# Kernel tuning notes

Hardware: AMD Instinct MI355X
Metric: run time of the kernel (lower is better)

Reference implementation:

```python
import jax, jax.numpy as jnp
import numpy as np

N = 50000
D_IN = 256
OUT = 16
HEADS = 32
GAT_C = OUT  # out_channels + beta_on(=0)


def _gat_conv(x, src, dst, W, att_src, att_dst, bias):
    """PyG GATConv, concat=False (mean over heads), with self-loops already appended."""
    n = x.shape[0]
    xp = (x @ W).reshape(n, HEADS, GAT_C)            # [N,H,C]
    a_s = jnp.einsum('nhc,hc->nh', xp, att_src)       # [N,H]
    a_d = jnp.einsum('nhc,hc->nh', xp, att_dst)       # [N,H]
    e = jax.nn.leaky_relu(a_s[src] + a_d[dst], 0.2)   # [E,H]
    # segment softmax over incoming edges of each dst node
    m = jax.ops.segment_max(e, dst, num_segments=n)
    e = jnp.exp(e - m[dst])
    s = jax.ops.segment_sum(e, dst, num_segments=n)
    alpha = e / (s[dst] + 1e-16)                      # [E,H]
    out = jax.ops.segment_sum(alpha[:, :, None] * xp[src], dst, num_segments=n)  # [N,H,C]
    return out.mean(axis=1) + bias                    # [N,C]


def setup_inputs() -> dict:
    key = jax.random.key(0)
    ks = jax.random.split(key, 16)
    E = 800000
    x = jax.random.normal(ks[0], (N, D_IN), dtype=jnp.float32)
    edge_index = jax.random.randint(ks[1], (2, E), 0, N, dtype=jnp.int64)
    sc = 1.0 / np.sqrt(D_IN)
    W1 = jax.random.normal(ks[2], (D_IN, HEADS * GAT_C), dtype=jnp.float32) * sc
    att_src1 = jax.random.normal(ks[3], (HEADS, GAT_C), dtype=jnp.float32) * 0.1
    att_dst1 = jax.random.normal(ks[4], (HEADS, GAT_C), dtype=jnp.float32) * 0.1
    b1 = jnp.zeros((GAT_C,), dtype=jnp.float32)
    W2 = jax.random.normal(ks[5], (D_IN, HEADS * GAT_C), dtype=jnp.float32) * sc
    att_src2 = jax.random.normal(ks[6], (HEADS, GAT_C), dtype=jnp.float32) * 0.1
    att_dst2 = jax.random.normal(ks[7], (HEADS, GAT_C), dtype=jnp.float32) * 0.1
    b2 = jnp.zeros((GAT_C,), dtype=jnp.float32)
    lin1_w = jax.random.normal(ks[8], (D_IN, 4 * OUT), dtype=jnp.float32) * sc
    lin1_b = jnp.zeros((4 * OUT,), dtype=jnp.float32)
    lin2_w = jax.random.normal(ks[9], (4 * OUT, OUT), dtype=jnp.float32) * (1.0 / np.sqrt(4 * OUT))
    lin2_b = jnp.zeros((OUT,), dtype=jnp.float32)
    return {"x": x, "edge_index": edge_index,
            "W1": W1, "att_src1": att_src1, "att_dst1": att_dst1, "b1": b1,
            "W2": W2, "att_src2": att_src2, "att_dst2": att_dst2, "b2": b2,
            "lin1_w": lin1_w, "lin1_b": lin1_b, "lin2_w": lin2_w, "lin2_b": lin2_b}


def reference(x, edge_index, W1, att_src1, att_dst1, b1, W2, att_src2, att_dst2, b2,
              lin1_w, lin1_b, lin2_w, lin2_b):
    n = x.shape[0]
    loops = jnp.arange(n, dtype=edge_index.dtype)
    # conv1: flow source_to_target on edge_index -> aggregate src=row0 into dst=row1
    src = jnp.concatenate([edge_index[0], loops])
    dst = jnp.concatenate([edge_index[1], loops])
    x_in = jax.nn.elu(_gat_conv(x, src, dst, W1, att_src1, att_dst1, b1))
    # conv2: flow target_to_source on transposed edge_index -> same effective (src,dst)
    x_out = jax.nn.elu(_gat_conv(x, src, dst, W2, att_src2, att_dst2, b2))
    x1 = jax.nn.elu(x @ lin1_w + lin1_b)
    x_self = jax.nn.elu(x1 @ lin2_w + lin2_b)
    return (x_in, x_out, x_self)
```

## Files before the change

### kernel.cpp

```cpp
#include <hip/hip_runtime.h>

typedef __bf16 bf16x8 __attribute__((ext_vector_type(8)));
typedef float  f32x4  __attribute__((ext_vector_type(4)));
typedef float  f32x2  __attribute__((ext_vector_type(2)));

#define NNODES   50000
#define DIN      256
#define HEADS    32
#define CDIM     16
#define NH       512
#define ERAW     800000
#define SCAN_B   196
#define LDSW     280
#define LOG2E    1.4426950408889634f
#define CAST_B   12500
#define PREP_B   (CAST_B + SCAN_B + 18)

#if __has_builtin(__builtin_amdgcn_exp2f)
#define EXP2(x) __builtin_amdgcn_exp2f(x)
#else
#define EXP2(x) __expf((x) * 0.6931471805599453f)
#endif

__device__ __forceinline__ float b2f(unsigned short u) {
    return __uint_as_float(((unsigned)u) << 16);
}
__device__ __forceinline__ unsigned short f2b(float f) {
    unsigned v = __float_as_uint(f);
    v += 0x7fffu + ((v >> 16) & 1u);
    return (unsigned short)(v >> 16);
}

__global__ void __launch_bounds__(256) k_prep(
        const float* __restrict__ x, unsigned short* __restrict__ xb,
        const float* __restrict__ W0, const float* __restrict__ W1,
        const float* __restrict__ w1, const float* __restrict__ w2,
        unsigned short* __restrict__ Wt2, unsigned short* __restrict__ w1t,
        unsigned short* __restrict__ w2t,
        const int* __restrict__ ei, int* __restrict__ flag,
        int* __restrict__ deg, int* __restrict__ cur) {
    __shared__ unsigned short T[64][258];
    int bid = blockIdx.x, t = threadIdx.x;

    if (bid < CAST_B) {
        int i = bid * 256 + t;
        float4 v = *(const float4*)(x + (size_t)i * 4);
        ushort4 o;
        o.x = f2b(v.x); o.y = f2b(v.y); o.z = f2b(v.z); o.w = f2b(v.w);
        *(ushort4*)(xb + (size_t)i * 4) = o;
        return;
    }
    if (bid < CAST_B + SCAN_B) {
        int i = (bid - CAST_B) * 256 + t;
        if (i < NNODES) { deg[i] = 0; cur[i] = 0; }
        if (bid == CAST_B && t == 0) {
            int nz = 0;
            #pragma unroll
            for (int k = 0; k < 64; ++k) nz |= ei[2 * k + 1];
            flag[0] = (nz == 0) ? 1 : 0;
        }
        return;
    }
    int tb = bid - (CAST_B + SCAN_B);
    if (tb == 17) {
        for (int idx = t; idx < 1024; idx += 256) {
            int n = idx >> 6, k = idx & 63;
            w2t[n * 64 + k] = f2b(w2[k * CDIM + n]);
        }
        return;
    }
    const float* src; unsigned short* dst; int srcStride, doPi, tile;
    if (tb < 8)       { src = W0; dst = Wt2;             srcStride = NH; doPi = 1; tile = tb; }
    else if (tb < 16) { src = W1; dst = Wt2 + 512 * DIN; srcStride = NH; doPi = 1; tile = tb - 8; }
    else              { src = w1; dst = w1t;             srcStride = 64; doPi = 0; tile = 0; }
    int n0 = tile * 64;
    int nl = (t & 15) * 4;
    int kr = t >> 4;
    for (int kk = 0; kk < 256; kk += 16) {
        int k = kk + kr;
        float4 v = *(const float4*)(src + (size_t)k * srcStride + n0 + nl);
        T[nl + 0][k] = f2b(v.x);
        T[nl + 1][k] = f2b(v.y);
        T[nl + 2][k] = f2b(v.z);
        T[nl + 3][k] = f2b(v.w);
    }
    __syncthreads();
    int rl = t >> 2;
    int pr = doPi ? (((rl & 15) << 2) | (rl >> 4)) : rl;
    #pragma unroll
    for (int j = 0; j < 16; ++j) {
        int c4 = (t & 3) + 4 * j;
        ushort2 o0 = *(const ushort2*)&T[pr][c4 * 4];
        ushort2 o1 = *(const ushort2*)&T[pr][c4 * 4 + 2];
        ushort4 o; o.x = o0.x; o.y = o0.y; o.z = o1.x; o.w = o1.y;
        *(ushort4*)(dst + ((size_t)(n0 + rl)) * DIN + c4 * 4) = o;
    }
}

__global__ void k_hist(const int* __restrict__ ei, const int* __restrict__ flag,
                       int* __restrict__ deg) {
    int e = blockIdx.x * 256 + threadIdx.x;
    int d = flag[0] ? ei[2 * ERAW + 2 * e] : ei[ERAW + e];
    atomicAdd(&deg[d], 1);
}

__global__ void k_scan_blk(const int* __restrict__ deg, int* __restrict__ part,
                           int* __restrict__ bsum) {
    __shared__ int sm[256];
    int b = blockIdx.x, t = threadIdx.x, i = b * 256 + t;
    int v = (i < NNODES) ? deg[i] : 0;
    sm[t] = v; __syncthreads();
    for (int off = 1; off < 256; off <<= 1) {
        int u = (t >= off) ? sm[t - off] : 0;
        __syncthreads();
        sm[t] += u; __syncthreads();
    }
    if (i < NNODES) part[i] = sm[t] - v;
    if (t == 255) bsum[b] = sm[255];
}

__global__ void k_scan_top(int* __restrict__ bsum) {
    __shared__ int sm[256];
    int t = threadIdx.x;
    int v = (t < SCAN_B) ? bsum[t] : 0;
    sm[t] = v; __syncthreads();
    for (int off = 1; off < 256; off <<= 1) {
        int u = (t >= off) ? sm[t - off] : 0;
        __syncthreads();
        sm[t] += u; __syncthreads();
    }
    if (t < SCAN_B) bsum[t] = sm[t] - v;
}

__global__ void k_scatter(const int* __restrict__ ei, const int* __restrict__ flag,
                          const int* __restrict__ part, const int* __restrict__ bsum,
                          int* __restrict__ cur, int* __restrict__ csr) {
    int e = blockIdx.x * 256 + threadIdx.x;
    int s, d;
    if (flag[0]) { s = ei[2 * e]; d = ei[2 * ERAW + 2 * e]; }
    else         { s = ei[e];     d = ei[ERAW + e]; }
    int pos = part[d] + bsum[d >> 8] + atomicAdd(&cur[d], 1);
    csr[pos] = s;
}

__global__ void __launch_bounds__(256)
k_gemm_xp(const unsigned short* __restrict__ xb,
          const unsigned short* __restrict__ Wt,
          unsigned* __restrict__ xp8,
          const float* __restrict__ att_src, const float* __restrict__ att_dst,
          float* __restrict__ a_s, float* __restrict__ a_d) {
    __shared__ unsigned short As[64 * LDSW];
    int row0 = blockIdx.x * 64;
    int tid = threadIdx.x;
    int w = tid >> 6, lane = tid & 63;
    int r = lane & 15, quad = lane >> 4;

    {
        int row = tid >> 2, slot = tid & 3;
        const uint4* g = (const uint4*)(xb + (size_t)(row0 + row) * DIN);
        uint4* l = (uint4*)(As + row * LDSW);
        #pragma unroll
        for (int i = 0; i < 8; ++i)
            l[slot + 4 * i] = g[slot + 4 * i];
    }
    __syncthreads();

    const f32x4* As4 = (const f32x4*)att_src;
    const f32x4* Ad4 = (const f32x4*)att_dst;

    #pragma unroll
    for (int ch = 0; ch < 2; ++ch) {
        f32x4 acc[4][4] = {};
        #pragma unroll
        for (int kc = 0; kc < 8; ++kc) {
            bf16x8 a[4], b[4];
            #pragma unroll
            for (int sub = 0; sub < 4; ++sub)
                a[sub] = *(const bf16x8*)(As + (sub * 16 + r) * LDSW + kc * 32 + quad * 8);
            #pragma unroll
            for (int t = 0; t < 4; ++t) {
                int col = ch * 256 + w * 64 + t * 16 + r;
                b[t] = *(const bf16x8*)(Wt + (size_t)col * DIN + kc * 32 + quad * 8);
            }
            #pragma unroll
            for (int t = 0; t < 4; ++t)
                #pragma unroll
                for (int sub = 0; sub < 4; ++sub)
                    acc[sub][t] = __builtin_amdgcn_mfma_f32_16x16x32_bf16(a[sub], b[t], acc[sub][t], 0, 0, 0);
        }
        int h = ch * 16 + w * 4 + (r >> 2);
        f32x4 sc = As4[h * 4 + (r & 3)];
        f32x4 dc = Ad4[h * 4 + (r & 3)];
        #pragma unroll
        for (int sub = 0; sub < 4; ++sub) {
            #pragma unroll
            for (int j = 0; j < 4; ++j) {
                int row = row0 + sub * 16 + quad * 4 + j;
                if (row < NNODES) {
                    unsigned u = (unsigned)__builtin_amdgcn_cvt_pk_fp8_f32(
                                     acc[sub][0][j], acc[sub][1][j], 0, false);
                    u = (unsigned)__builtin_amdgcn_cvt_pk_fp8_f32(
                                     acc[sub][2][j], acc[sub][3][j], (int)u, true);
                    xp8[(size_t)row * 128 + ch * 64 + w * 16 + r] = u;
                }
            }
            f32x4 ps = acc[sub][0] * sc.x + acc[sub][1] * sc.y
                     + acc[sub][2] * sc.z + acc[sub][3] * sc.w;
            f32x4 pd = acc[sub][0] * dc.x + acc[sub][1] * dc.y
                     + acc[sub][2] * dc.z + acc[sub][3] * dc.w;
            #pragma unroll
            for (int m = 1; m <= 2; m <<= 1) {
                #pragma unroll
                for (int c = 0; c < 4; ++c) {
                    ps[c] += __shfl_xor(ps[c], m, 64);
                    pd[c] += __shfl_xor(pd[c], m, 64);
                }
            }
            int j = r & 3;
            int row = row0 + sub * 16 + quad * 4 + j;
            if (row < NNODES) {
                a_s[row * HEADS + h] = ps[j] * LOG2E;
                a_d[row * HEADS + h] = pd[j] * LOG2E;
            }
        }
    }
}

__global__ void k_conv(const int* __restrict__ csr, const int* __restrict__ part,
                       const int* __restrict__ bsum, const int* __restrict__ deg,
                       const unsigned* __restrict__ xp8,
                       const float* __restrict__ a_s, const float* __restrict__ a_d,
                       const float* __restrict__ bias, float* __restrict__ out) {
    int nd = blockIdx.x * 4 + (threadIdx.x >> 6);
    int ln = threadIdx.x & 63;
    int h  = ln >> 1;
    int cb = (ln & 1) * 8;
    float adn = a_d[nd * HEADS + h];
    int beg = __builtin_amdgcn_readfirstlane(part[nd])
            + __builtin_amdgcn_readfirstlane(bsum[nd >> 8]);
    int cnt = __builtin_amdgcn_readfirstlane(deg[nd]);
    const uint2* xv = (const uint2*)xp8;

    float denom = 0.f;
    float acc[8] = {0, 0, 0, 0, 0, 0, 0, 0};

    #define EDGE_BODY(AV, QV, LIVE)                                        \
    {                                                                      \
        float tt = (AV) + adn;                                             \
        tt = fmaxf(tt, 0.2f * tt);                                         \
        float e = EXP2(tt);                                                \
        e = (LIVE) ? e : 0.f;                                              \
        denom += e;                                                        \
        f32x2 p0 = __builtin_amdgcn_cvt_pk_f32_fp8((int)(QV).x, false);    \
        f32x2 p1 = __builtin_amdgcn_cvt_pk_f32_fp8((int)(QV).x, true);     \
        f32x2 p2 = __builtin_amdgcn_cvt_pk_f32_fp8((int)(QV).y, false);    \
        f32x2 p3 = __builtin_amdgcn_cvt_pk_f32_fp8((int)(QV).y, true);     \
        acc[0] += e * p0.x; acc[1] += e * p0.y;                            \
        acc[2] += e * p1.x; acc[3] += e * p1.y;                            \
        acc[4] += e * p2.x; acc[5] += e * p2.y;                            \
        acc[6] += e * p3.x; acc[7] += e * p3.y;                            \
    }

    float avS = a_s[nd * HEADS + h];
    uint2 qvS = xv[(size_t)nd * 64 + ln];
    int nb = (cnt + 3) >> 2;
    float avP[4]; uint2 qvP[4]; int svN[4];
    if (nb > 0) {
        #pragma unroll
        for (int k = 0; k < 4; ++k) {
            int ce = k < cnt ? k : cnt - 1;
            int s = csr[beg + ce];
            avP[k] = a_s[s * HEADS + h];
            qvP[k] = xv[(size_t)s * 64 + ln];
        }
        #pragma unroll
        for (int k = 0; k < 4; ++k) {
            int idx = 4 + k;
            int ce = idx < cnt ? idx : cnt - 1;
            svN[k] = csr[beg + ce];
        }
    }
    __builtin_amdgcn_sched_barrier(0);
    EDGE_BODY(avS, qvS, 1)

    for (int b = 1; b < nb; ++b) {
        float avN[4]; uint2 qvN[4];
        #pragma unroll
        for (int k = 0; k < 4; ++k) {
            int s = svN[k];
            avN[k] = a_s[s * HEADS + h];
            qvN[k] = xv[(size_t)s * 64 + ln];
        }
        {
            int nbase = (b + 1 < nb ? b + 1 : nb - 1) * 4;
            #pragma unroll
            for (int k = 0; k < 4; ++k) {
                int idx = nbase + k;
                int ce = idx < cnt ? idx : cnt - 1;
                svN[k] = csr[beg + ce];
            }
        }
        __builtin_amdgcn_sched_barrier(0);
        #pragma unroll
        for (int k = 0; k < 4; ++k) EDGE_BODY(avP[k], qvP[k], 1)
        #pragma unroll
        for (int k = 0; k < 4; ++k) { avP[k] = avN[k]; qvP[k] = qvN[k]; }
    }
    if (nb > 0) {
        #pragma unroll
        for (int k = 0; k < 4; ++k) {
            int idx = (nb - 1) * 4 + k;
            EDGE_BODY(avP[k], qvP[k], idx < cnt)
        }
    }
    #undef EDGE_BODY

    float inv = 1.f / (denom + 1e-16f);
    #pragma unroll
    for (int c = 0; c < 8; ++c) acc[c] *= inv;

    #pragma unroll
    for (int mask = 2; mask <= 32; mask <<= 1) {
        #pragma unroll
        for (int c = 0; c < 8; ++c) acc[c] += __shfl_xor(acc[c], mask, 64);
    }
    if (ln < 2) {
        #pragma unroll
        for (int c2 = 0; c2 < 8; ++c2) {
            int c = cb + c2;
            float o = acc[c2] * (1.0f / HEADS) + bias[c];
            out[(size_t)nd * CDIM + c] = o > 0.f ? o : expm1f(o);
        }
    }
}

__global__ void __launch_bounds__(256)
k_mlp(const unsigned short* __restrict__ xb, const unsigned short* __restrict__ w1t,
      const float* __restrict__ bb1, const unsigned short* __restrict__ w2t,
      const float* __restrict__ bb2, float* __restrict__ out) {
    __shared__ unsigned short T[4][64][72];
    int wv = threadIdx.x >> 6;
    int wave = blockIdx.x * 4 + wv;
    if (wave >= 782) return;
    int lane = threadIdx.x & 63;
    int r = lane & 15, quad = lane >> 4;
    int row0 = wave * 64;

    f32x4 acc[4][4] = {};
    #pragma unroll
    for (int kc = 0; kc < 8; ++kc) {
        bf16x8 a[4];
        #pragma unroll
        for (int sub = 0; sub < 4; ++sub) {
            int row = row0 + sub * 16 + r;
            if (row0 + sub * 16 < NNODES)
                a[sub] = *(const bf16x8*)(xb + (size_t)row * DIN + kc * 32 + quad * 8);
            else {
                union { unsigned short u[8]; bf16x8 v; } z;
                #pragma unroll
                for (int j = 0; j < 8; ++j) z.u[j] = 0;
                a[sub] = z.v;
            }
        }
        #pragma unroll
        for (int t = 0; t < 4; ++t) {
            int col = t * 16 + r;
            bf16x8 b = *(const bf16x8*)(w1t + (size_t)col * DIN + kc * 32 + quad * 8);
            #pragma unroll
            for (int sub = 0; sub < 4; ++sub)
                acc[sub][t] = __builtin_amdgcn_mfma_f32_16x16x32_bf16(a[sub], b, acc[sub][t], 0, 0, 0);
        }
    }
    #pragma unroll
    for (int sub = 0; sub < 4; ++sub) {
        #pragma unroll
        for (int t = 0; t < 4; ++t) {
            int col = t * 16 + r;
            float bv = bb1[col];
            #pragma unroll
            for (int j = 0; j < 4; ++j) {
                float v = acc[sub][t][j] + bv;
                v = v > 0.f ? v : expm1f(v);
                T[wv][sub * 16 + quad * 4 + j][col] = f2b(v);
            }
        }
    }
    f32x4 acc2[4] = {};
    #pragma unroll
    for (int sub = 0; sub < 4; ++sub) {
        #pragma unroll
        for (int kc = 0; kc < 2; ++kc) {
            bf16x8 a = *(const bf16x8*)&T[wv][sub * 16 + r][kc * 32 + quad * 8];
            bf16x8 b = *(const bf16x8*)(w2t + r * 64 + kc * 32 + quad * 8);
            acc2[sub] = __builtin_amdgcn_mfma_f32_16x16x32_bf16(a, b, acc2[sub], 0, 0, 0);
        }
    }
    float bv2 = bb2[r];
    #pragma unroll
    for (int sub = 0; sub < 4; ++sub) {
        #pragma unroll
        for (int j = 0; j < 4; ++j) {
            int row = row0 + sub * 16 + quad * 4 + j;
            if (row < NNODES) {
                float v = acc2[sub][j] + bv2;
                out[(size_t)row * CDIM + r] = v > 0.f ? v : expm1f(v);
            }
        }
    }
}

extern "C" void kernel_launch(void* const* d_in, const int* in_sizes, int n_in,
                              void* d_out, int out_size, void* d_ws, size_t ws_size,
                              hipStream_t stream) {
    const float* x  = (const float*)d_in[0];
    const int* ei   = (const int*)d_in[1];
    const float* W[2]    = {(const float*)d_in[2], (const float*)d_in[6]};
    const float* atS[2]  = {(const float*)d_in[3], (const float*)d_in[7]};
    const float* atD[2]  = {(const float*)d_in[4], (const float*)d_in[8]};
    const float* bias[2] = {(const float*)d_in[5], (const float*)d_in[9]};
    const float* w1 = (const float*)d_in[10];
    const float* b1 = (const float*)d_in[11];
    const float* w2 = (const float*)d_in[12];
    const float* b2 = (const float*)d_in[13];
    float* out = (float*)d_out;

    char* ws = (char*)d_ws;
    unsigned* xp8 = (unsigned*)(ws);
    unsigned short* xb  = (unsigned short*)(ws + 25600000);
    unsigned short* Wt2 = (unsigned short*)(ws + 51200000);
    unsigned short* w1t = (unsigned short*)(ws + 51724288);
    unsigned short* w2t = (unsigned short*)(ws + 51757056);
    float* a_s = (float*)(ws + 51759104);
    float* a_d = (float*)(ws + 58159104);
    int* deg   = (int*)(ws + 64559104);
    int* cur   = (int*)(ws + 64759104);
    int* part  = (int*)(ws + 64959104);
    int* bsum  = (int*)(ws + 65159104);
    int* csr   = (int*)(ws + 65160128);
    int* flag  = (int*)(ws + 68360128);

    k_prep    <<<PREP_B, 256, 0, stream>>>(x, xb, W[0], W[1], w1, w2,
                                           Wt2, w1t, w2t, ei, flag, deg, cur);
    k_hist    <<<3125, 256, 0, stream>>>(ei, flag, deg);
    k_scan_blk<<<SCAN_B, 256, 0, stream>>>(deg, part, bsum);
    k_scan_top<<<1, 256, 0, stream>>>(bsum);
    k_scatter <<<3125, 256, 0, stream>>>(ei, flag, part, bsum, cur, csr);

    for (int cv = 0; cv < 2; ++cv) {
        k_gemm_xp<<<782, 256, 0, stream>>>(xb, Wt2 + (size_t)cv * 512 * DIN,
                                           xp8, atS[cv], atD[cv], a_s, a_d);
        k_conv   <<<12500, 256, 0, stream>>>(csr, part, bsum, deg, xp8, a_s, a_d,
                                             bias[cv], out + (size_t)cv * 800000);
    }
    k_mlp<<<196, 256, 0, stream>>>(xb, w1t, b1, w2t, b2, out + 1600000);
}
```

Measured before the change: 461.2 us.

## Merge GEMMs, histogram and MLP into one launch; fuse both convs and scan

Independent work (both GAT projection GEMMs, the degree histogram, and the MLP branch) now runs as block ranges of a single k_mix launch, so small kernels can overlap and fill the GPU. Both conv layers run in one 25000-block launch using separate xp8/a_s/a_d buffers. The two-level scan is merged into one kernel where the last-finishing block does the top-level scan, tracked by an atomic counter. This needs a larger workspace, so the old sequential path is kept as a fallback when the workspace is too small.

After: 445.9 us. -3.3%, faster.

```diff
diff --git a/kernel.cpp b/kernel.cpp
--- a/kernel.cpp
+++ b/kernel.cpp
@@ -15,6 +15,10 @@
 #define LOG2E    1.4426950408889634f
 #define CAST_B   12500
 #define PREP_B   (CAST_B + SCAN_B + 18)
+#define GEMM_B   782
+#define HIST_B   3125
+#define MLP_B    196
+#define MIX_B    (2 * GEMM_B + HIST_B + MLP_B)
 
 #if __has_builtin(__builtin_amdgcn_exp2f)
 #define EXP2(x) __builtin_amdgcn_exp2f(x)
@@ -58,6 +62,7 @@
             #pragma unroll
             for (int k = 0; k < 64; ++k) nz |= ei[2 * k + 1];
             flag[0] = (nz == 0) ? 1 : 0;
+            flag[1] = 0;
         }
         return;
     }
@@ -97,16 +102,222 @@
     }
 }
 
+__device__ __forceinline__ void hist_body(int bid, int t,
+        const int* __restrict__ ei, const int* __restrict__ flag,
+        int* __restrict__ deg) {
+    int e = bid * 256 + t;
+    int d = flag[0] ? ei[2 * ERAW + 2 * e] : ei[ERAW + e];
+    atomicAdd(&deg[d], 1);
+}
+
+__device__ __forceinline__ void gemm_body(int bid, int tid,
+        const unsigned short* __restrict__ xb,
+        const unsigned short* __restrict__ Wt,
+        unsigned* __restrict__ xp8,
+        const float* __restrict__ att_src, const float* __restrict__ att_dst,
+        float* __restrict__ a_s, float* __restrict__ a_d,
+        unsigned short* As) {
+    int row0 = bid * 64;
+    int w = tid >> 6, lane = tid & 63;
+    int r = lane & 15, quad = lane >> 4;
+
+    {
+        int row = tid >> 2, slot = tid & 3;
+        const uint4* g = (const uint4*)(xb + (size_t)(row0 + row) * DIN);
+        uint4* l = (uint4*)(As + row * LDSW);
+        #pragma unroll
+        for (int i = 0; i < 8; ++i)
+            l[slot + 4 * i] = g[slot + 4 * i];
+    }
+    __syncthreads();
+
+    const f32x4* As4 = (const f32x4*)att_src;
+    const f32x4* Ad4 = (const f32x4*)att_dst;
+
+    #pragma unroll
+    for (int ch = 0; ch < 2; ++ch) {
+        f32x4 acc[4][4] = {};
+        #pragma unroll
+        for (int kc = 0; kc < 8; ++kc) {
+            bf16x8 a[4], b[4];
+            #pragma unroll
+            for (int sub = 0; sub < 4; ++sub)
+                a[sub] = *(const bf16x8*)(As + (sub * 16 + r) * LDSW + kc * 32 + quad * 8);
+            #pragma unroll
+            for (int t = 0; t < 4; ++t) {
+                int col = ch * 256 + w * 64 + t * 16 + r;
+                b[t] = *(const bf16x8*)(Wt + (size_t)col * DIN + kc * 32 + quad * 8);
+            }
+            #pragma unroll
+            for (int t = 0; t < 4; ++t)
+                #pragma unroll
+                for (int sub = 0; sub < 4; ++sub)
+                    acc[sub][t] = __builtin_amdgcn_mfma_f32_16x16x32_bf16(a[sub], b[t], acc[sub][t], 0, 0, 0);
+        }
+        int h = ch * 16 + w * 4 + (r >> 2);
+        f32x4 sc = As4[h * 4 + (r & 3)];
+        f32x4 dc = Ad4[h * 4 + (r & 3)];
+        #pragma unroll
+        for (int sub = 0; sub < 4; ++sub) {
+            #pragma unroll
+            for (int j = 0; j < 4; ++j) {
+                int row = row0 + sub * 16 + quad * 4 + j;
+                if (row < NNODES) {
+                    unsigned u = (unsigned)__builtin_amdgcn_cvt_pk_fp8_f32(
+                                     acc[sub][0][j], acc[sub][1][j], 0, false);
+                    u = (unsigned)__builtin_amdgcn_cvt_pk_fp8_f32(
+                                     acc[sub][2][j], acc[sub][3][j], (int)u, true);
+                    xp8[(size_t)row * 128 + ch * 64 + w * 16 + r] = u;
+                }
+            }
+            f32x4 ps = acc[sub][0] * sc.x + acc[sub][1] * sc.y
+                     + acc[sub][2] * sc.z + acc[sub][3] * sc.w;
+            f32x4 pd = acc[sub][0] * dc.x + acc[sub][1] * dc.y
+                     + acc[sub][2] * dc.z + acc[sub][3] * dc.w;
+            #pragma unroll
+            for (int m = 1; m <= 2; m <<= 1) {
+                #pragma unroll
+                for (int c = 0; c < 4; ++c) {
+                    ps[c] += __shfl_xor(ps[c], m, 64);
+                    pd[c] += __shfl_xor(pd[c], m, 64);
+                }
+            }
+            int j = r & 3;
+            int row = row0 + sub * 16 + quad * 4 + j;
+            if (row < NNODES) {
+                a_s[row * HEADS + h] = ps[j] * LOG2E;
+                a_d[row * HEADS + h] = pd[j] * LOG2E;
+            }
+        }
+    }
+}
+
+__device__ __forceinline__ void mlp_body(int bid, int tid,
+        const unsigned short* __restrict__ xb, const unsigned short* __restrict__ w1t,
+        const float* __restrict__ bb1, const unsigned short* __restrict__ w2t,
+        const float* __restrict__ bb2, float* __restrict__ out,
+        unsigned short* Tbase) {
+    int wv = tid >> 6;
+    int wave = bid * 4 + wv;
+    if (wave >= GEMM_B) return;
+    unsigned short* T = Tbase + wv * 64 * 72;
+    int lane = tid & 63;
+    int r = lane & 15, quad = lane >> 4;
+    int row0 = wave * 64;
+
+    f32x4 acc[4][4] = {};
+    #pragma unroll
+    for (int kc = 0; kc < 8; ++kc) {
+        bf16x8 a[4];
+        #pragma unroll
+        for (int sub = 0; sub < 4; ++sub) {
+            int row = row0 + sub * 16 + r;
+            if (row0 + sub * 16 < NNODES)
+                a[sub] = *(const bf16x8*)(xb + (size_t)row * DIN + kc * 32 + quad * 8);
+            else {
+                union { unsigned short u[8]; bf16x8 v; } z;
+                #pragma unroll
+                for (int j = 0; j < 8; ++j) z.u[j] = 0;
+                a[sub] = z.v;
+            }
+        }
+        #pragma unroll
+        for (int t = 0; t < 4; ++t) {
+            int col = t * 16 + r;
+            bf16x8 b = *(const bf16x8*)(w1t + (size_t)col * DIN + kc * 32 + quad * 8);
+            #pragma unroll
+            for (int sub = 0; sub < 4; ++sub)
+                acc[sub][t] = __builtin_amdgcn_mfma_f32_16x16x32_bf16(a[sub], b, acc[sub][t], 0, 0, 0);
+        }
+    }
+    #pragma unroll
+    for (int sub = 0; sub < 4; ++sub) {
+        #pragma unroll
+        for (int t = 0; t < 4; ++t) {
+            int col = t * 16 + r;
+            float bv = bb1[col];
+            #pragma unroll
+            for (int j = 0; j < 4; ++j) {
+                float v = acc[sub][t][j] + bv;
+                v = v > 0.f ? v : expm1f(v);
+                T[(sub * 16 + quad * 4 + j) * 72 + col] = f2b(v);
+            }
+        }
+    }
+    f32x4 acc2[4] = {};
+    #pragma unroll
+    for (int sub = 0; sub < 4; ++sub) {
+        #pragma unroll
+        for (int kc = 0; kc < 2; ++kc) {
+            bf16x8 a = *(const bf16x8*)&T[(sub * 16 + r) * 72 + kc * 32 + quad * 8];
+            bf16x8 b = *(const bf16x8*)(w2t + r * 64 + kc * 32 + quad * 8);
+            acc2[sub] = __builtin_amdgcn_mfma_f32_16x16x32_bf16(a, b, acc2[sub], 0, 0, 0);
+        }
+    }
+    float bv2 = bb2[r];
+    #pragma unroll
+    for (int sub = 0; sub < 4; ++sub) {
+        #pragma unroll
+        for (int j = 0; j < 4; ++j) {
+            int row = row0 + sub * 16 + quad * 4 + j;
+            if (row < NNODES) {
+                float v = acc2[sub][j] + bv2;
+                out[(size_t)row * CDIM + r] = v > 0.f ? v : expm1f(v);
+            }
+        }
+    }
+}
+
 __global__ void k_hist(const int* __restrict__ ei, const int* __restrict__ flag,
                        int* __restrict__ deg) {
-    int e = blockIdx.x * 256 + threadIdx.x;
-    int d = flag[0] ? ei[2 * ERAW + 2 * e] : ei[ERAW + e];
-    atomicAdd(&deg[d], 1);
-}
-
-__global__ void k_scan_blk(const int* __restrict__ deg, int* __restrict__ part,
-                           int* __restrict__ bsum) {
+    hist_body(blockIdx.x, threadIdx.x, ei, flag, deg);
+}
+
+__global__ void __launch_bounds__(256)
+k_gemm_xp(const unsigned short* __restrict__ xb, const unsigned short* __restrict__ Wt,
+          unsigned* __restrict__ xp8,
+          const float* __restrict__ atS, const float* __restrict__ atD,
+          float* __restrict__ a_s, float* __restrict__ a_d) {
+    __shared__ unsigned short As[64 * LDSW];
+    gemm_body(blockIdx.x, threadIdx.x, xb, Wt, xp8, atS, atD, a_s, a_d, As);
+}
+
+__global__ void __launch_bounds__(256)
+k_mlp(const unsigned short* __restrict__ xb, const unsigned short* __restrict__ w1t,
+      const float* __restrict__ bb1, const unsigned short* __restrict__ w2t,
+      const float* __restrict__ bb2, float* __restrict__ out) {
+    __shared__ unsigned short T[4 * 64 * 72];
+    mlp_body(blockIdx.x, threadIdx.x, xb, w1t, bb1, w2t, bb2, out, T);
+}
+
+__global__ void __launch_bounds__(256) k_mix(
+        const unsigned short* __restrict__ xb, const unsigned short* __restrict__ Wt2,
+        unsigned* __restrict__ xp8_0, unsigned* __restrict__ xp8_1,
+        const float* __restrict__ atS0, const float* __restrict__ atD0,
+        const float* __restrict__ atS1, const float* __restrict__ atD1,
+        float* __restrict__ as0, float* __restrict__ ad0,
+        float* __restrict__ as1, float* __restrict__ ad1,
+        const int* __restrict__ ei, const int* __restrict__ flag,
+        int* __restrict__ deg,
+        const unsigned short* __restrict__ w1t, const float* __restrict__ b1,
+        const unsigned short* __restrict__ w2t, const float* __restrict__ b2,
+        float* __restrict__ outm) {
+    __shared__ unsigned short SH[4 * 64 * 72];
+    int bid = blockIdx.x, tid = threadIdx.x;
+    if (bid < GEMM_B)
+        gemm_body(bid, tid, xb, Wt2, xp8_0, atS0, atD0, as0, ad0, SH);
+    else if (bid < 2 * GEMM_B)
+        gemm_body(bid - GEMM_B, tid, xb, Wt2 + 512 * DIN, xp8_1, atS1, atD1, as1, ad1, SH);
+    else if (bid < 2 * GEMM_B + HIST_B)
+        hist_body(bid - 2 * GEMM_B, tid, ei, flag, deg);
+    else
+        mlp_body(bid - (2 * GEMM_B + HIST_B), tid, xb, w1t, b1, w2t, b2, outm, SH);
+}
+
+__global__ void k_scan(const int* __restrict__ deg, int* __restrict__ part,
+                       int* __restrict__ bsum, int* __restrict__ done) {
     __shared__ int sm[256];
+    __shared__ int isLast;
     int b = blockIdx.x, t = threadIdx.x, i = b * 256 + t;
     int v = (i < NNODES) ? deg[i] : 0;
     sm[t] = v; __syncthreads();
@@ -117,19 +328,20 @@
     }
     if (i < NNODES) part[i] = sm[t] - v;
     if (t == 255) bsum[b] = sm[255];
-}
-
-__global__ void k_scan_top(int* __restrict__ bsum) {
-    __shared__ int sm[256];
-    int t = threadIdx.x;
-    int v = (t < SCAN_B) ? bsum[t] : 0;
-    sm[t] = v; __syncthreads();
-    for (int off = 1; off < 256; off <<= 1) {
-        int u = (t >= off) ? sm[t - off] : 0;
-        __syncthreads();
-        sm[t] += u; __syncthreads();
-    }
-    if (t < SCAN_B) bsum[t] = sm[t] - v;
+    __threadfence();
+    if (t == 0) isLast = (atomicAdd(done, 1) == SCAN_B - 1);
+    __syncthreads();
+    if (isLast) {
+        __threadfence();
+        int v2 = (t < SCAN_B) ? bsum[t] : 0;
+        sm[t] = v2; __syncthreads();
+        for (int off = 1; off < 256; off <<= 1) {
+            int u = (t >= off) ? sm[t - off] : 0;
+            __syncthreads();
+            sm[t] += u; __syncthreads();
+        }
+        if (t < SCAN_B) bsum[t] = sm[t] - v2;
+    }
 }
 
 __global__ void k_scatter(const int* __restrict__ ei, const int* __restrict__ flag,
@@ -144,94 +356,20 @@
 }
 
 __global__ void __launch_bounds__(256)
-k_gemm_xp(const unsigned short* __restrict__ xb,
-          const unsigned short* __restrict__ Wt,
-          unsigned* __restrict__ xp8,
-          const float* __restrict__ att_src, const float* __restrict__ att_dst,
-          float* __restrict__ a_s, float* __restrict__ a_d) {
-    __shared__ unsigned short As[64 * LDSW];
-    int row0 = blockIdx.x * 64;
-    int tid = threadIdx.x;
-    int w = tid >> 6, lane = tid & 63;
-    int r = lane & 15, quad = lane >> 4;
-
-    {
-        int row = tid >> 2, slot = tid & 3;
-        const uint4* g = (const uint4*)(xb + (size_t)(row0 + row) * DIN);
-        uint4* l = (uint4*)(As + row * LDSW);
-        #pragma unroll
-        for (int i = 0; i < 8; ++i)
-            l[slot + 4 * i] = g[slot + 4 * i];
-    }
-    __syncthreads();
-
-    const f32x4* As4 = (const f32x4*)att_src;
-    const f32x4* Ad4 = (const f32x4*)att_dst;
-
-    #pragma unroll
-    for (int ch = 0; ch < 2; ++ch) {
-        f32x4 acc[4][4] = {};
-        #pragma unroll
-        for (int kc = 0; kc < 8; ++kc) {
-            bf16x8 a[4], b[4];
-            #pragma unroll
-            for (int sub = 0; sub < 4; ++sub)
-                a[sub] = *(const bf16x8*)(As + (sub * 16 + r) * LDSW + kc * 32 + quad * 8);
-            #pragma unroll
-            for (int t = 0; t < 4; ++t) {
-                int col = ch * 256 + w * 64 + t * 16 + r;
-                b[t] = *(const bf16x8*)(Wt + (size_t)col * DIN + kc * 32 + quad * 8);
-            }
-            #pragma unroll
-            for (int t = 0; t < 4; ++t)
-                #pragma unroll
-                for (int sub = 0; sub < 4; ++sub)
-                    acc[sub][t] = __builtin_amdgcn_mfma_f32_16x16x32_bf16(a[sub], b[t], acc[sub][t], 0, 0, 0);
-        }
-        int h = ch * 16 + w * 4 + (r >> 2);
-        f32x4 sc = As4[h * 4 + (r & 3)];
-        f32x4 dc = Ad4[h * 4 + (r & 3)];
-        #pragma unroll
-        for (int sub = 0; sub < 4; ++sub) {
-            #pragma unroll
-            for (int j = 0; j < 4; ++j) {
-                int row = row0 + sub * 16 + quad * 4 + j;
-                if (row < NNODES) {
-                    unsigned u = (unsigned)__builtin_amdgcn_cvt_pk_fp8_f32(
-                                     acc[sub][0][j], acc[sub][1][j], 0, false);
-                    u = (unsigned)__builtin_amdgcn_cvt_pk_fp8_f32(
-                                     acc[sub][2][j], acc[sub][3][j], (int)u, true);
-                    xp8[(size_t)row * 128 + ch * 64 + w * 16 + r] = u;
-                }
-            }
-            f32x4 ps = acc[sub][0] * sc.x + acc[sub][1] * sc.y
-                     + acc[sub][2] * sc.z + acc[sub][3] * sc.w;
-            f32x4 pd = acc[sub][0] * dc.x + acc[sub][1] * dc.y
-                     + acc[sub][2] * dc.z + acc[sub][3] * dc.w;
-            #pragma unroll
-            for (int m = 1; m <= 2; m <<= 1) {
-                #pragma unroll
-                for (int c = 0; c < 4; ++c) {
-                    ps[c] += __shfl_xor(ps[c], m, 64);
-                    pd[c] += __shfl_xor(pd[c], m, 64);
-                }
-            }
-            int j = r & 3;
-            int row = row0 + sub * 16 + quad * 4 + j;
-            if (row < NNODES) {
-                a_s[row * HEADS + h] = ps[j] * LOG2E;
-                a_d[row * HEADS + h] = pd[j] * LOG2E;
-            }
-        }
-    }
-}
-
-__global__ void k_conv(const int* __restrict__ csr, const int* __restrict__ part,
-                       const int* __restrict__ bsum, const int* __restrict__ deg,
-                       const unsigned* __restrict__ xp8,
-                       const float* __restrict__ a_s, const float* __restrict__ a_d,
-                       const float* __restrict__ bias, float* __restrict__ out) {
-    int nd = blockIdx.x * 4 + (threadIdx.x >> 6);
+k_conv(const int* __restrict__ csr, const int* __restrict__ part,
+       const int* __restrict__ bsum, const int* __restrict__ deg,
+       const unsigned* __restrict__ xp8A, const float* __restrict__ asA,
+       const float* __restrict__ adA, const float* __restrict__ biasA,
+       float* __restrict__ outA,
+       const unsigned* __restrict__ xp8B, const float* __restrict__ asB,
+       const float* __restrict__ adB, const float* __restrict__ biasB,
+       float* __restrict__ outB, int nsplit) {
+    int bid = blockIdx.x;
+    const unsigned* xp8; const float* a_s; const float* a_d;
+    const float* bias; float* out; int b0;
+    if (bid < nsplit) { xp8 = xp8A; a_s = asA; a_d = adA; bias = biasA; out = outA; b0 = bid; }
+    else              { xp8 = xp8B; a_s = asB; a_d = adB; bias = biasB; out = outB; b0 = bid - nsplit; }
+    int nd = b0 * 4 + (threadIdx.x >> 6);
     int ln = threadIdx.x & 63;
     int h  = ln >> 1;
     int cb = (ln & 1) * 8;
@@ -334,81 +472,6 @@
     }
 }
 
-__global__ void __launch_bounds__(256)
-k_mlp(const unsigned short* __restrict__ xb, const unsigned short* __restrict__ w1t,
-      const float* __restrict__ bb1, const unsigned short* __restrict__ w2t,
-      const float* __restrict__ bb2, float* __restrict__ out) {
-    __shared__ unsigned short T[4][64][72];
-    int wv = threadIdx.x >> 6;
-    int wave = blockIdx.x * 4 + wv;
-    if (wave >= 782) return;
-    int lane = threadIdx.x & 63;
-    int r = lane & 15, quad = lane >> 4;
-    int row0 = wave * 64;
-
-    f32x4 acc[4][4] = {};
-    #pragma unroll
-    for (int kc = 0; kc < 8; ++kc) {
-        bf16x8 a[4];
-        #pragma unroll
-        for (int sub = 0; sub < 4; ++sub) {
-            int row = row0 + sub * 16 + r;
-            if (row0 + sub * 16 < NNODES)
-                a[sub] = *(const bf16x8*)(xb + (size_t)row * DIN + kc * 32 + quad * 8);
-            else {
-                union { unsigned short u[8]; bf16x8 v; } z;
-                #pragma unroll
-                for (int j = 0; j < 8; ++j) z.u[j] = 0;
-                a[sub] = z.v;
-            }
-        }
-        #pragma unroll
-        for (int t = 0; t < 4; ++t) {
-            int col = t * 16 + r;
-            bf16x8 b = *(const bf16x8*)(w1t + (size_t)col * DIN + kc * 32 + quad * 8);
-            #pragma unroll
-            for (int sub = 0; sub < 4; ++sub)
-                acc[sub][t] = __builtin_amdgcn_mfma_f32_16x16x32_bf16(a[sub], b, acc[sub][t], 0, 0, 0);
-        }
-    }
-    #pragma unroll
-    for (int sub = 0; sub < 4; ++sub) {
-        #pragma unroll
-        for (int t = 0; t < 4; ++t) {
-            int col = t * 16 + r;
-            float bv = bb1[col];
-            #pragma unroll
-            for (int j = 0; j < 4; ++j) {
-                float v = acc[sub][t][j] + bv;
-                v = v > 0.f ? v : expm1f(v);
-                T[wv][sub * 16 + quad * 4 + j][col] = f2b(v);
-            }
-        }
-    }
-    f32x4 acc2[4] = {};
-    #pragma unroll
-    for (int sub = 0; sub < 4; ++sub) {
-        #pragma unroll
-        for (int kc = 0; kc < 2; ++kc) {
-            bf16x8 a = *(const bf16x8*)&T[wv][sub * 16 + r][kc * 32 + quad * 8];
-            bf16x8 b = *(const bf16x8*)(w2t + r * 64 + kc * 32 + quad * 8);
-            acc2[sub] = __builtin_amdgcn_mfma_f32_16x16x32_bf16(a, b, acc2[sub], 0, 0, 0);
-        }
-    }
-    float bv2 = bb2[r];
-    #pragma unroll
-    for (int sub = 0; sub < 4; ++sub) {
-        #pragma unroll
-        for (int j = 0; j < 4; ++j) {
-            int row = row0 + sub * 16 + quad * 4 + j;
-            if (row < NNODES) {
-                float v = acc2[sub][j] + bv2;
-                out[(size_t)row * CDIM + r] = v > 0.f ? v : expm1f(v);
-            }
-        }
-    }
-}
-
 extern "C" void kernel_launch(void* const* d_in, const int* in_sizes, int n_in,
                               void* d_out, int out_size, void* d_ws, size_t ws_size,
                               hipStream_t stream) {
@@ -423,34 +486,69 @@
     const float* w2 = (const float*)d_in[12];
     const float* b2 = (const float*)d_in[13];
     float* out = (float*)d_out;
-
     char* ws = (char*)d_ws;
-    unsigned* xp8 = (unsigned*)(ws);
-    unsigned short* xb  = (unsigned short*)(ws + 25600000);
-    unsigned short* Wt2 = (unsigned short*)(ws + 51200000);
-    unsigned short* w1t = (unsigned short*)(ws + 51724288);
-    unsigned short* w2t = (unsigned short*)(ws + 51757056);
-    float* a_s = (float*)(ws + 51759104);
-    float* a_d = (float*)(ws + 58159104);
-    int* deg   = (int*)(ws + 64559104);
-    int* cur   = (int*)(ws + 64759104);
-    int* part  = (int*)(ws + 64959104);
-    int* bsum  = (int*)(ws + 65159104);
-    int* csr   = (int*)(ws + 65160128);
-    int* flag  = (int*)(ws + 68360128);
-
-    k_prep    <<<PREP_B, 256, 0, stream>>>(x, xb, W[0], W[1], w1, w2,
-                                           Wt2, w1t, w2t, ei, flag, deg, cur);
-    k_hist    <<<3125, 256, 0, stream>>>(ei, flag, deg);
-    k_scan_blk<<<SCAN_B, 256, 0, stream>>>(deg, part, bsum);
-    k_scan_top<<<1, 256, 0, stream>>>(bsum);
-    k_scatter <<<3125, 256, 0, stream>>>(ei, flag, part, bsum, cur, csr);
-
-    for (int cv = 0; cv < 2; ++cv) {
-        k_gemm_xp<<<782, 256, 0, stream>>>(xb, Wt2 + (size_t)cv * 512 * DIN,
-                                           xp8, atS[cv], atD[cv], a_s, a_d);
-        k_conv   <<<12500, 256, 0, stream>>>(csr, part, bsum, deg, xp8, a_s, a_d,
-                                             bias[cv], out + (size_t)cv * 800000);
-    }
-    k_mlp<<<196, 256, 0, stream>>>(xb, w1t, b1, w2t, b2, out + 1600000);
-}
+
+    const size_t NEED_BIG = 106760192;
+    if (ws_size >= NEED_BIG) {
+        unsigned* xp8_0 = (unsigned*)(ws);
+        unsigned* xp8_1 = (unsigned*)(ws + 25600000);
+        unsigned short* xb  = (unsigned short*)(ws + 51200000);
+        unsigned short* Wt2 = (unsigned short*)(ws + 76800000);
+        unsigned short* w1t = (unsigned short*)(ws + 77324288);
+        unsigned short* w2t = (unsigned short*)(ws + 77357056);
+        float* as0 = (float*)(ws + 77359104);
+        float* ad0 = (float*)(ws + 83759104);
+        float* as1 = (float*)(ws + 90159104);
+        float* ad1 = (float*)(ws + 96559104);
+        int* deg   = (int*)(ws + 102959104);
+        int* cur   = (int*)(ws + 103159104);
+        int* part  = (int*)(ws + 103359104);
+        int* bsum  = (int*)(ws + 103559104);
+        int* flag  = (int*)(ws + 103560128);
+        int* csr   = (int*)(ws + 103560192);
+
+        k_prep   <<<PREP_B, 256, 0, stream>>>(x, xb, W[0], W[1], w1, w2,
+                                              Wt2, w1t, w2t, ei, flag, deg, cur);
+        k_mix    <<<MIX_B, 256, 0, stream>>>(xb, Wt2, xp8_0, xp8_1,
+                                             atS[0], atD[0], atS[1], atD[1],
+                                             as0, ad0, as1, ad1,
+                                             ei, flag, deg,
+                                             w1t, b1, w2t, b2, out + 1600000);
+        k_scan   <<<SCAN_B, 256, 0, stream>>>(deg, part, bsum, flag + 1);
+        k_scatter<<<3125, 256, 0, stream>>>(ei, flag, part, bsum, cur, csr);
+        k_conv   <<<25000, 256, 0, stream>>>(csr, part, bsum, deg,
+                                             xp8_0, as0, ad0, bias[0], out,
+                                             xp8_1, as1, ad1, bias[1], out + 800000,
+                                             12500);
+    } else {
+        unsigned* xp8 = (unsigned*)(ws);
+        unsigned short* xb  = (unsigned short*)(ws + 25600000);
+        unsigned short* Wt2 = (unsigned short*)(ws + 51200000);
+        unsigned short* w1t = (unsigned short*)(ws + 51724288);
+        unsigned short* w2t = (unsigned short*)(ws + 51757056);
+        float* a_s = (float*)(ws + 51759104);
+        float* a_d = (float*)(ws + 58159104);
+        int* deg   = (int*)(ws + 64559104);
+        int* cur   = (int*)(ws + 64759104);
+        int* part  = (int*)(ws + 64959104);
+        int* bsum  = (int*)(ws + 65159104);
+        int* csr   = (int*)(ws + 65160128);
+        int* flag  = (int*)(ws + 68360128);
+
+        k_prep   <<<PREP_B, 256, 0, stream>>>(x, xb, W[0], W[1], w1, w2,
+                                              Wt2, w1t, w2t, ei, flag, deg, cur);
+        k_hist   <<<HIST_B, 256, 0, stream>>>(ei, flag, deg);
+        k_scan   <<<SCAN_B, 256, 0, stream>>>(deg, part, bsum, flag + 1);
+        k_scatter<<<3125, 256, 0, stream>>>(ei, flag, part, bsum, cur, csr);
+        for (int cv = 0; cv < 2; ++cv) {
+            k_gemm_xp<<<GEMM_B, 256, 0, stream>>>(xb, Wt2 + (size_t)cv * 512 * DIN,
+                                                  xp8, atS[cv], atD[cv], a_s, a_d);
+            k_conv   <<<12500, 256, 0, stream>>>(csr, part, bsum, deg,
+                                                 xp8, a_s, a_d, bias[cv],
+                                                 out + (size_t)cv * 800000,
+                                                 xp8, a_s, a_d, bias[cv],
+                                                 out + (size_t)cv * 800000, 12500);
+        }
+        k_mlp<<<MLP_B, 256, 0, stream>>>(xb, w1t, b1, w2t, b2, out + 1600000);
+    }
+}
```
